# Optimization experiments

Measured on AMD Instinct MI355X. Metric: run time of the kernel, lower is better.

The kernel has to match this reference:

```python
import jax, jax.numpy as jnp
import numpy as np

ALPHA = 0.1
EPS = 1e-8


def _segment_mean_std(feats, idx, num_segments):
    # feats: (N, C), idx: (N,) int -> mean/std per segment, torch.std is unbiased (ddof=1)
    ones = jnp.ones((feats.shape[0],), feats.dtype)
    cnt = jax.ops.segment_sum(ones, idx, num_segments=num_segments)  # (B,)
    ssum = jax.ops.segment_sum(feats, idx, num_segments=num_segments)  # (B, C)
    mean = ssum / cnt[:, None]
    diff = feats - mean[idx]
    var = jax.ops.segment_sum(diff * diff, idx, num_segments=num_segments) / (cnt[:, None] - 1.0)
    std = jnp.sqrt(jnp.maximum(var, 0.0)) + EPS
    return mean, std


def _adain(content_feats, style_feats, content_batch_indices, style_batch_indices, num_batches):
    c_mean, c_std = _segment_mean_std(content_feats, content_batch_indices, num_batches)
    s_mean, s_std = _segment_mean_std(style_feats, style_batch_indices, num_batches)
    # sequential EMA of global stats across batch ids (globals start as first batch's style stats)
    g0 = jnp.concatenate([s_mean[:1], s_std[:1]], axis=0)  # (2, C)
    rest = jnp.stack([s_mean[1:], s_std[1:]], axis=1)  # (B-1, 2, C)

    def step(g, s):
        g_new = (1.0 - ALPHA) * g + ALPHA * s
        return g_new, g_new

    _, g_rest = jax.lax.scan(step, g0, rest)
    g_all = jnp.concatenate([g0[None], g_rest], axis=0)  # (B, 2, C)
    g_mean, g_std = g_all[:, 0], g_all[:, 1]  # (B, C) each
    # per-row gather + normalize (each batch uses globals AFTER its own update)
    ci = content_batch_indices
    return g_std[ci] * (content_feats - c_mean[ci]) / c_std[ci] + g_mean[ci]


def setup_inputs() -> dict:
    key = jax.random.key(0)
    k1, k2, k3, k4 = jax.random.split(key, 4)
    N_c, N_s, C, B = 1000000, 250000, 64, 16
    return {
        "content_feats": jax.random.normal(k1, (N_c, C), dtype=jnp.float32),
        "style_feats": jax.random.normal(k2, (N_s, C), dtype=jnp.float32),
        "content_batch_indices": jax.random.randint(k3, (N_c,), 0, B, dtype=jnp.int32),
        "style_batch_indices": jax.random.randint(k4, (N_s,), 0, B, dtype=jnp.int32),
        "num_batches": B,
    }


def reference(content_feats, style_feats, content_batch_indices, style_batch_indices, num_batches):
    return _adain(content_feats, style_feats, content_batch_indices, style_batch_indices, num_batches)
```

## Files before the change

### kernel.cpp

```cpp
#include <hip/hip_runtime.h>


#define NB 16
#define NC 64
#define NREP 16
#define CBLKS 1228
#define SBLKS 308

typedef float fvec4 __attribute__((ext_vector_type(4)));
typedef float f32x4 __attribute__((ext_vector_type(4)));
typedef short bf16x8 __attribute__((ext_vector_type(8)));

#define WS_CPART 0
#define WS_SPART (NREP * 2048)
#define WS_CCNT  (2 * NREP * 2048)
#define WS_SCNT  (WS_CCNT + NREP * NB)
#define WS_SCALE (WS_SCNT + NREP * NB)
#define WS_BIAS  (WS_SCALE + 1024)
#define WS_ZERO_FLOATS WS_SCALE

__device__ __forceinline__ unsigned cvtpk(float lo, float hi)
{
    unsigned r;
    asm("v_cvt_pk_bf16_f32 %0, %1, %2" : "=v"(r) : "v"(lo), "v"(hi));
    return r;
}

__device__ __forceinline__ void gload16(const float* g, float* l)
{
    __builtin_amdgcn_global_load_lds(
        (const __attribute__((address_space(1))) void*)g,
        (__attribute__((address_space(3))) void*)l, 16, 0, 0);
}

__device__ __forceinline__ void stage_tile(
    const float* __restrict__ feats, int nrows, int rb, int wv, int lane,
    float* bufp)
{
    #pragma unroll
    for (int u = 0; u < 2; ++u) {
        const int i = 2 * wv + u;
        int rg = rb + i * 4 + (lane >> 4);
        if (rg > nrows - 1) rg = nrows - 1;
        const int c4 = (lane & 15) ^ (2 * ((i >> 1) & 3));
        gload16(feats + (size_t)rg * NC + c4 * 4, bufp + i * 256);
    }
}

__device__ __forceinline__ void reduce_body(
    const float* __restrict__ feats, const int* __restrict__ idx, int nrows,
    float* __restrict__ part, float* __restrict__ cntp,
    int blk, int nblk, int tid, float* buf , float* lsum )
{
    const int lane = tid & 63;
    const int wv   = tid >> 6;
    const int half = lane >> 4;
    const int sub  = lane & 15;

    f32x4 accS = {0, 0, 0, 0}, accQ = {0, 0, 0, 0};
    int cnti = 0;

    const int ntiles = (nrows + 31) >> 5;
    const int tpb = (ntiles + nblk - 1) / nblk;
    const int t0 = blk * tpb;
    const int t1 = (t0 + tpb < ntiles) ? (t0 + tpb) : ntiles;

    const int c4p   = (wv * 4 + (sub >> 2)) ^ (2 * half);
    const int rbase = half * 8 * NC + c4p * 4 + (sub & 3);

    int vidx = -1;
    if (t0 < t1) {
        stage_tile(feats, nrows, t0 << 5, wv, lane, buf);
        const int rl = (t0 << 5) + (lane & 31);
        vidx = (rl < nrows) ? idx[rl] : -1;
    }

    int cur = 0;
    for (int t = t0; t < t1; ++t) {
        __syncthreads();

        if (t + 1 < t1)
            stage_tile(feats, nrows, (t + 1) << 5, wv, lane, buf + (cur ^ 1) * 2048);
        int vn = -1;
        if (t + 1 < t1) {
            const int rl = ((t + 1) << 5) + (lane & 31);
            vn = (rl < nrows) ? idx[rl] : -1;
        }

        #pragma unroll
        for (int bb = 0; bb < 4; ++bb) {
            const int b = wv * 4 + bb;
            const unsigned long long m = __ballot(vidx == b) & 0xFFFFFFFFull;
            cnti += (lane == b) ? (int)__popcll(m) : 0;
        }

        union { unsigned w[4]; bf16x8 v; } A;
        const int kb4 = half * 32;
        #pragma unroll
        for (int i = 0; i < 4; ++i) {
            const int k0 = __builtin_amdgcn_ds_bpermute(kb4 + 8 * i,     vidx);
            const int k1 = __builtin_amdgcn_ds_bpermute(kb4 + 8 * i + 4, vidx);
            const unsigned lo = (k0 == sub) ? 0x3F80u     : 0u;
            const unsigned hi = (k1 == sub) ? 0x3F800000u : 0u;
            A.w[i] = lo | hi;
        }

        const float* bp = buf + cur * 2048;
        float xv[8];
        #pragma unroll
        for (int j = 0; j < 8; ++j)
            xv[j] = bp[rbase + j * NC];

        union { unsigned w[4]; bf16x8 v; } Bs, Bq;
        #pragma unroll
        for (int i = 0; i < 4; ++i) {
            const float a0 = xv[2 * i], a1 = xv[2 * i + 1];
            Bs.w[i] = cvtpk(a0, a1);
            Bq.w[i] = cvtpk(a0 * a0, a1 * a1);
        }

        accS = __builtin_amdgcn_mfma_f32_16x16x32_bf16(A.v, Bs.v, accS, 0, 0, 0);
        accQ = __builtin_amdgcn_mfma_f32_16x16x32_bf16(A.v, Bq.v, accQ, 0, 0, 0);

        vidx = vn;
        cur ^= 1;
    }

    #pragma unroll
    for (int i = 0; i < 4; ++i) {
        const int m = half * 4 + i;
        lsum[m * NC + wv * 16 + sub]        = accS[i];
        lsum[1024 + m * NC + wv * 16 + sub] = accQ[i];
    }
    __syncthreads();
    float* dst = part + (blk & (NREP - 1)) * 2048;
    for (int i = tid; i < 2048; i += 256)
        atomicAdd(&dst[i], lsum[i]);
    if ((lane >> 2) == wv && lane < NB)
        atomicAdd(&cntp[(blk & (NREP - 1)) * NB + lane], (float)cnti);
}

__global__ __launch_bounds__(256) void reduce_stats(
    const float* __restrict__ content, const int* __restrict__ ci, int Nc,
    const float* __restrict__ style,   const int* __restrict__ si, int Ns,
    float* __restrict__ ws)
{
    __shared__ float buf[2 * 2048];
    __shared__ float lsum[2048];
    if (blockIdx.x < CBLKS)
        reduce_body(content, ci, Nc, ws + WS_CPART, ws + WS_CCNT,
                    blockIdx.x, CBLKS, threadIdx.x, buf, lsum);
    else
        reduce_body(style, si, Ns, ws + WS_SPART, ws + WS_SCNT,
                    blockIdx.x - CBLKS, SBLKS, threadIdx.x, buf, lsum);
}

__global__ void finalize_kernel(float* __restrict__ ws)
{
    if (threadIdx.x >= NC) return;
    const int c = threadIdx.x;
    const float* c_part = ws + WS_CPART;
    const float* s_part = ws + WS_SPART;
    const float* c_cntp = ws + WS_CCNT;
    const float* s_cntp = ws + WS_SCNT;
    float* scale = ws + WS_SCALE;
    float* bias  = ws + WS_BIAS;

    float gm = 0.f, gs = 0.f;
    for (int b = 0; b < NB; ++b) {
        float csum = 0.f, csq = 0.f, ssum = 0.f, ssq = 0.f, ccnt = 0.f, scnt = 0.f;
        #pragma unroll
        for (int rep = 0; rep < NREP; ++rep) {
            csum += c_part[rep * 2048 + b * NC + c];
            csq  += c_part[rep * 2048 + 1024 + b * NC + c];
            ssum += s_part[rep * 2048 + b * NC + c];
            ssq  += s_part[rep * 2048 + 1024 + b * NC + c];
            ccnt += c_cntp[rep * NB + b];
            scnt += s_cntp[rep * NB + b];
        }
        const float smean = ssum / scnt;
        const float svar  = (ssq - scnt * smean * smean) / (scnt - 1.0f);
        const float sstd  = sqrtf(fmaxf(svar, 0.f)) + 1e-8f;
        if (b == 0) { gm = smean; gs = sstd; }
        else        { gm = 0.9f * gm + 0.1f * smean; gs = 0.9f * gs + 0.1f * sstd; }
        const float cmean = csum / ccnt;
        const float cvar  = (csq - ccnt * cmean * cmean) / (ccnt - 1.0f);
        const float cstd  = sqrtf(fmaxf(cvar, 0.f)) + 1e-8f;
        const float sc = gs / cstd;
        scale[b * NC + c] = sc;
        bias [b * NC + c] = gm - sc * cmean;
    }
}

__global__ __launch_bounds__(256) void apply_kernel(
    const float* __restrict__ content, const int* __restrict__ ci, int Nc,
    const float* __restrict__ ws, fvec4* __restrict__ out4)
{
    __shared__ fvec4 s_sc[NB * 17];
    __shared__ fvec4 s_bi[NB * 17];
    const fvec4* scale4 = (const fvec4*)(ws + WS_SCALE);
    const fvec4* bias4  = (const fvec4*)(ws + WS_BIAS);
    for (int i = threadIdx.x; i < NB * 16; i += 256) {
        const int b = i >> 4, c4 = i & 15;
        s_sc[b * 17 + c4] = scale4[i];
        s_bi[b * 17 + c4] = bias4[i];
    }
    __syncthreads();

    const fvec4* feats4 = (const fvec4*)content;
    const int total4 = Nc * 16;
    const int stride = gridDim.x * 256;
    for (int i = blockIdx.x * 256 + threadIdx.x; i < total4; i += stride) {
        const int r  = i >> 4;
        const int c4 = i & 15;
        const int b  = ci[r];
        const fvec4 v  = feats4[i];
        const fvec4 sc = s_sc[b * 17 + c4];
        const fvec4 bi = s_bi[b * 17 + c4];
        fvec4 o;
        o.x = fmaf(sc.x, v.x, bi.x);
        o.y = fmaf(sc.y, v.y, bi.y);
        o.z = fmaf(sc.z, v.z, bi.z);
        o.w = fmaf(sc.w, v.w, bi.w);
        __builtin_nontemporal_store(o, &out4[i]);
    }
}

extern "C" void kernel_launch(void* const* d_in, const int* in_sizes, int n_in,
                              void* d_out, int out_size, void* d_ws, size_t ws_size,
                              hipStream_t stream)
{
    const float* content = (const float*)d_in[0];
    const float* style   = (const float*)d_in[1];
    const int*   ci      = (const int*)d_in[2];
    const int*   si      = (const int*)d_in[3];

    const int Nc = in_sizes[0] / NC;
    const int Ns = in_sizes[1] / NC;

    float* ws = (float*)d_ws;
    (void)hipMemsetAsync(ws, 0, WS_ZERO_FLOATS * sizeof(float), stream);

    reduce_stats<<<CBLKS + SBLKS, 256, 0, stream>>>(content, ci, Nc, style, si, Ns, ws);
    finalize_kernel<<<1, 64, 0, stream>>>(ws);
    apply_kernel<<<2048, 256, 0, stream>>>(content, ci, Nc, ws, (fvec4*)d_out);
}
```

Before: 185.1 us.

## Triple-buffer reduction staging with explicit vmcnt waits and fewer blocks

Replaces the double-buffered LDS staging loop in the stats reduction with a three-stage ring buffer. Each stage waits on a partial vmcnt instead of a full syncthreads, so up to two tiles stay in flight while one is consumed. Index loads are clamped so they can be issued unconditionally. Grid sizes drop to 1024 content and 256 style blocks, which gives each block more tiles and raises LDS use to 32 KB per block. This may lower occupancy, and the hand-placed waitcnt and barriers are fragile to get right.

```diff
diff --git a/kernel.cpp b/kernel.cpp
--- a/kernel.cpp
+++ b/kernel.cpp
@@ -4,8 +4,8 @@
 #define NB 16
 #define NC 64
 #define NREP 16
-#define CBLKS 1228
-#define SBLKS 308
+#define CBLKS 1024
+#define SBLKS 256
 
 typedef float fvec4 __attribute__((ext_vector_type(4)));
 typedef float f32x4 __attribute__((ext_vector_type(4)));
@@ -47,6 +47,15 @@
     }
 }
 
+__device__ __forceinline__ int idx_load(
+    const int* __restrict__ idx, int nrows, int ct, int lane)
+{
+    const int rl = (ct << 5) + (lane & 31);
+    int rc = rl; if (rc > nrows - 1) rc = nrows - 1;
+    const int raw = idx[rc];
+    return (rl < nrows) ? raw : -1;
+}
+
 __device__ __forceinline__ void reduce_body(
     const float* __restrict__ feats, const int* __restrict__ idx, int nrows,
     float* __restrict__ part, float* __restrict__ cntp,
@@ -68,63 +77,72 @@
     const int c4p   = (wv * 4 + (sub >> 2)) ^ (2 * half);
     const int rbase = half * 8 * NC + c4p * 4 + (sub & 3);
 
-    int vidx = -1;
+#define CLAMPT(x) (((x) < t1) ? (x) : (t1 - 1))
+
+#define CONSUME(bi, vv) do {                                                 \
+        asm volatile("s_waitcnt vmcnt(7)" ::: "memory");                     \
+        __builtin_amdgcn_sched_barrier(0);                                   \
+        __builtin_amdgcn_s_barrier();                                        \
+        __builtin_amdgcn_sched_barrier(0);                                   \
+        _Pragma("unroll")                                                    \
+        for (int bb = 0; bb < 4; ++bb) {                                     \
+            const int b = wv * 4 + bb;                                       \
+            const unsigned long long m = __ballot((vv) == b) & 0xFFFFFFFFull;\
+            cnti += (lane == b) ? (int)__popcll(m) : 0;                      \
+        }                                                                    \
+        union { unsigned w[4]; bf16x8 v; } A;                                \
+        const int kb4 = half * 32;                                           \
+        _Pragma("unroll")                                                    \
+        for (int i = 0; i < 4; ++i) {                                        \
+            const int k0 = __builtin_amdgcn_ds_bpermute(kb4 + 8 * i,     (vv));\
+            const int k1 = __builtin_amdgcn_ds_bpermute(kb4 + 8 * i + 4, (vv));\
+            const unsigned lo = (k0 == sub) ? 0x3F80u     : 0u;              \
+            const unsigned hi = (k1 == sub) ? 0x3F800000u : 0u;              \
+            A.w[i] = lo | hi;                                                \
+        }                                                                    \
+        const float* bp = buf + (bi) * 2048;                                 \
+        float xv[8];                                                         \
+        _Pragma("unroll")                                                    \
+        for (int j = 0; j < 8; ++j) xv[j] = bp[rbase + j * NC];              \
+        union { unsigned w[4]; bf16x8 v; } Bs, Bq;                           \
+        _Pragma("unroll")                                                    \
+        for (int i = 0; i < 4; ++i) {                                        \
+            const float a0 = xv[2 * i], a1 = xv[2 * i + 1];                  \
+            Bs.w[i] = cvtpk(a0, a1);                                         \
+            Bq.w[i] = cvtpk(a0 * a0, a1 * a1);                               \
+        }                                                                    \
+        accS = __builtin_amdgcn_mfma_f32_16x16x32_bf16(A.v, Bs.v, accS, 0, 0, 0);\
+        accQ = __builtin_amdgcn_mfma_f32_16x16x32_bf16(A.v, Bq.v, accQ, 0, 0, 0);\
+        __builtin_amdgcn_sched_barrier(0);                                   \
+        __builtin_amdgcn_s_barrier();         \
+        __builtin_amdgcn_sched_barrier(0);                                   \
+    } while (0)
+
+#define STAGE3(bi, vv, tcur) do {                                            \
+        const int ct = CLAMPT((tcur) + 3);                                   \
+        stage_tile(feats, nrows, ct << 5, wv, lane, buf + (bi) * 2048);      \
+        (vv) = idx_load(idx, nrows, ct, lane);                               \
+    } while (0)
+
     if (t0 < t1) {
+        int v0, v1, v2;
         stage_tile(feats, nrows, t0 << 5, wv, lane, buf);
-        const int rl = (t0 << 5) + (lane & 31);
-        vidx = (rl < nrows) ? idx[rl] : -1;
-    }
-
-    int cur = 0;
-    for (int t = t0; t < t1; ++t) {
-        __syncthreads();
-
-        if (t + 1 < t1)
-            stage_tile(feats, nrows, (t + 1) << 5, wv, lane, buf + (cur ^ 1) * 2048);
-        int vn = -1;
-        if (t + 1 < t1) {
-            const int rl = ((t + 1) << 5) + (lane & 31);
-            vn = (rl < nrows) ? idx[rl] : -1;
+        v0 = idx_load(idx, nrows, t0, lane);
+        stage_tile(feats, nrows, CLAMPT(t0 + 1) << 5, wv, lane, buf + 2048);
+        v1 = idx_load(idx, nrows, CLAMPT(t0 + 1), lane);
+        stage_tile(feats, nrows, CLAMPT(t0 + 2) << 5, wv, lane, buf + 4096);
+        v2 = idx_load(idx, nrows, CLAMPT(t0 + 2), lane);
+
+        int t = t0;
+        for (;;) {
+            CONSUME(0, v0); STAGE3(0, v0, t); if (++t >= t1) break;
+            CONSUME(1, v1); STAGE3(1, v1, t); if (++t >= t1) break;
+            CONSUME(2, v2); STAGE3(2, v2, t); if (++t >= t1) break;
         }
-
-        #pragma unroll
-        for (int bb = 0; bb < 4; ++bb) {
-            const int b = wv * 4 + bb;
-            const unsigned long long m = __ballot(vidx == b) & 0xFFFFFFFFull;
-            cnti += (lane == b) ? (int)__popcll(m) : 0;
-        }
-
-        union { unsigned w[4]; bf16x8 v; } A;
-        const int kb4 = half * 32;
-        #pragma unroll
-        for (int i = 0; i < 4; ++i) {
-            const int k0 = __builtin_amdgcn_ds_bpermute(kb4 + 8 * i,     vidx);
-            const int k1 = __builtin_amdgcn_ds_bpermute(kb4 + 8 * i + 4, vidx);
-            const unsigned lo = (k0 == sub) ? 0x3F80u     : 0u;
-            const unsigned hi = (k1 == sub) ? 0x3F800000u : 0u;
-            A.w[i] = lo | hi;
-        }
-
-        const float* bp = buf + cur * 2048;
-        float xv[8];
-        #pragma unroll
-        for (int j = 0; j < 8; ++j)
-            xv[j] = bp[rbase + j * NC];
-
-        union { unsigned w[4]; bf16x8 v; } Bs, Bq;
-        #pragma unroll
-        for (int i = 0; i < 4; ++i) {
-            const float a0 = xv[2 * i], a1 = xv[2 * i + 1];
-            Bs.w[i] = cvtpk(a0, a1);
-            Bq.w[i] = cvtpk(a0 * a0, a1 * a1);
-        }
-
-        accS = __builtin_amdgcn_mfma_f32_16x16x32_bf16(A.v, Bs.v, accS, 0, 0, 0);
-        accQ = __builtin_amdgcn_mfma_f32_16x16x32_bf16(A.v, Bq.v, accQ, 0, 0, 0);
-
-        vidx = vn;
-        cur ^= 1;
-    }
+    }
+#undef CONSUME
+#undef STAGE3
+#undef CLAMPT
 
     #pragma unroll
     for (int i = 0; i < 4; ++i) {
@@ -145,7 +163,7 @@
     const float* __restrict__ style,   const int* __restrict__ si, int Ns,
     float* __restrict__ ws)
 {
-    __shared__ float buf[2 * 2048];
+    __shared__ float buf[3 * 2048];
     __shared__ float lsum[2048];
     if (blockIdx.x < CBLKS)
         reduce_body(content, ci, Nc, ws + WS_CPART, ws + WS_CCNT,
```

Result: slower. 194.3 us (+5.0%).
